# Kernel optimization log

Hardware: AMD Instinct MI355X
Metric: run time of the kernel (lower is better)

## Reference

```python
import jax, jax.numpy as jnp
import numpy as np

R, N, E, IN_DIM, HID, SEM_H = 3, 50000, 500000, 256, 128, 128


def setup_inputs() -> dict:
    key = jax.random.key(0)
    ks = jax.random.split(key, 20)
    s = 0.05
    return {
        # forward tensor args
        "dst_feat": jax.random.normal(ks[0], (N, IN_DIM), jnp.float32),
        "src_feats": jax.random.normal(ks[1], (R, N, IN_DIM), jnp.float32),
        "src_idx": jax.random.randint(ks[2], (R, E), 0, N, jnp.int32),
        "dst_idx": jax.random.randint(ks[3], (R, E), 0, N, jnp.int32),
        # weight_T: per-ntype projection in_dim -> hidden (dst ntype + R src ntypes, stacked)
        "WT_dst": jax.random.normal(ks[4], (IN_DIM, HID), jnp.float32) * s,
        "bT_dst": jnp.zeros((HID,), jnp.float32),
        "WT_src": jax.random.normal(ks[5], (R, IN_DIM, HID), jnp.float32) * s,
        "bT_src": jnp.zeros((R, HID), jnp.float32),
        # GATConv params per relation (1 head, shared fc for src/dst since in_feats is int)
        "W_gat": jax.random.normal(ks[6], (R, HID, HID), jnp.float32) * s,
        "attn_l": jax.random.normal(ks[7], (R, HID), jnp.float32) * s,
        "attn_r": jax.random.normal(ks[8], (R, HID), jnp.float32) * s,
        "b_gat": jnp.zeros((R, HID), jnp.float32),
        # SemanticAttention: Linear(HID,128)+tanh+Linear(128,1,no bias)
        "W1_sem": jax.random.normal(ks[9], (HID, SEM_H), jnp.float32) * s,
        "b1_sem": jnp.zeros((SEM_H,), jnp.float32),
        "w2_sem": jax.random.normal(ks[10], (SEM_H, 1), jnp.float32) * s,
    }


def reference(dst_feat, src_feats, src_idx, dst_idx,
              WT_dst, bT_dst, WT_src, bT_src,
              W_gat, attn_l, attn_r, b_gat,
              W1_sem, b1_sem, w2_sem):
    # weight_T projections (raw feat dim != hidden_dim branch)
    h_dst = dst_feat @ WT_dst + bT_dst                                  # [N, H]
    h_src = jnp.einsum('rni,rio->rno', src_feats, WT_src) + bT_src[:, None, :]  # [R, N, H]
    n_nodes = h_dst.shape[0]

    def gat(h_s_in, si, di, W, al, ar, b):
        # DGL GATConv, 1 head, eval mode (no dropout), shared fc for src/dst
        hs = h_s_in @ W                                                 # [N, H]
        hd = h_dst @ W                                                  # [N, H]
        el = (hs * al).sum(-1)                                          # [N]
        er = (hd * ar).sum(-1)                                          # [N]
        e = el[si] + er[di]                                             # [E]
        e = jnp.where(e > 0, e, 0.2 * e)                                # leaky_relu(0.2)
        # edge softmax segmented by destination node
        m = jax.ops.segment_max(e, di, num_segments=n_nodes)
        ex = jnp.exp(e - m[di])
        ssum = jax.ops.segment_sum(ex, di, num_segments=n_nodes)
        alpha = ex / ssum[di]                                           # [E]
        out = jax.ops.segment_sum(alpha[:, None] * hs[si], di, num_segments=n_nodes)  # [N, H]
        return jax.nn.elu(out + b)                                      # activation=F.elu, + bias

    z_r = jax.vmap(gat)(h_src, src_idx, dst_idx, W_gat, attn_l, attn_r, b_gat)  # [R, N, H]

    # SemanticAttention over relations
    z_m = jnp.transpose(z_r, (1, 0, 2))                                 # [N, R, H]
    w = jnp.tanh(z_m @ W1_sem + b1_sem) @ w2_sem                        # [N, R, 1]
    a = jax.nn.softmax(w.mean(axis=0), axis=0)                          # [R, 1]
    return (z_m * a).sum(axis=1)                                        # [N, H]
```

## Files before the change

kernel.cpp:

```cpp
#include <hip/hip_runtime.h>
#include <hip/hip_bf16.h>

#define R_REL 3
#define NODE_CHUNK 512
#define BCAP 6144

typedef __attribute__((ext_vector_type(8))) short bf16x8;
typedef __attribute__((ext_vector_type(4))) float f32x4;

static inline size_t align_up(size_t x, size_t a) { return (x + a - 1) & ~(a - 1); }

__device__ __forceinline__ float eluf(float x) {
    return x > 0.f ? x : (__expf(x) - 1.f);
}
__device__ __forceinline__ unsigned short f2bf(float f) {
    __hip_bfloat16 h = __float2bfloat16(f);
    return *reinterpret_cast<unsigned short*>(&h);
}
__device__ __forceinline__ unsigned pk2bf(float lo, float hi) {
    __hip_bfloat162 h = __float22bfloat162_rn(make_float2(lo, hi));
    return *reinterpret_cast<unsigned*>(&h);
}
__device__ __forceinline__ float bf2f(unsigned short h) {
    return __uint_as_float((unsigned)h << 16);
}


__global__ void vu_kernel(const float* __restrict__ W_gat, const float* __restrict__ attn_r,
                          const float* __restrict__ WT_dst, const float* __restrict__ bT_dst,
                          float* __restrict__ u, float* __restrict__ cc) {
    int r = blockIdx.x;
    int t = threadIdx.x;
    __shared__ float ar[128];
    __shared__ float vs[128];
    if (t < 128) ar[t] = attn_r[r * 128 + t];
    __syncthreads();
    if (t < 128) {
        const float* W = W_gat + (size_t)r * 128 * 128 + (size_t)t * 128;
        float s = 0.f;
        for (int j = 0; j < 128; ++j) s += W[j] * ar[j];
        vs[t] = s;
    }
    __syncthreads();
    const float* W = WT_dst + (size_t)t * 128;
    float s = 0.f;
    for (int i = 0; i < 128; ++i) s += W[i] * vs[i];
    u[r * 256 + t] = s;
    if (t == 0) {
        float c = 0.f;
        for (int i = 0; i < 128; ++i) c += bT_dst[i] * vs[i];
        cc[r] = c;
    }
}

__global__ void wc_kernel(const float* __restrict__ WT_src, const float* __restrict__ bT_src,
                          const float* __restrict__ W_gat, float* __restrict__ Wc,
                          float* __restrict__ bc) {
    int r = blockIdx.y;
    int k = blockIdx.x;
    int j = threadIdx.x;
    __shared__ float as[128];
    const float* arow = (k < 256) ? (WT_src + ((size_t)r * 256 + k) * 128)
                                  : (bT_src + (size_t)r * 128);
    as[j] = arow[j];
    __syncthreads();
    const float* W = W_gat + (size_t)r * 128 * 128;
    float s = 0.f;
    for (int i = 0; i < 128; ++i) s += as[i] * W[(size_t)i * 128 + j];
    if (k < 256) Wc[((size_t)r * 256 + k) * 128 + j] = s;
    else         bc[(size_t)r * 128 + j] = s;
}

__global__ void pack_kernel(const float* __restrict__ S, unsigned short* __restrict__ P,
                            int relstride, int KS) {
    int r = blockIdx.y;
    int ks = blockIdx.x >> 3, cb = blockIdx.x & 7;
    int l = threadIdx.x;
    const float* Sr = S + (size_t)r * relstride;
    int col = cb * 16 + (l & 15);
    int kb = ks * 32 + (l >> 4) * 8;
    unsigned short v[8];
#pragma unroll
    for (int j = 0; j < 8; ++j) v[j] = f2bf(Sr[(size_t)(kb + j) * 128 + col]);
    unsigned short* dst = P + ((((size_t)r * KS + ks) * 8 + cb) * 64 + l) * 8;
    *(uint4*)dst = *(uint4*)v;
}


__global__ __launch_bounds__(512) void gemm_hs(
    const float* __restrict__ src, const unsigned short* __restrict__ Bpack,
    const float* __restrict__ bc, const float* __restrict__ attn_l,
    unsigned short* __restrict__ hsb, float* __restrict__ el, int N) {
    const int r = blockIdx.y;
    const int t = threadIdx.x;
    const int w = t >> 6, l = t & 63;
    __shared__ unsigned short Blds[256 * 128];

    const unsigned short* bsrc = Bpack + (size_t)r * 256 * 128;
#pragma unroll
    for (int i = 0; i < 8; ++i) {
        int c = i * 512 + t;
        *(uint4*)&Blds[(size_t)c * 8] = *(const uint4*)&bsrc[(size_t)c * 8];
    }
    __syncthreads();

    const int rowbase = blockIdx.x * 128 + w * 16;
    const int arow_i = rowbase + (l & 15);
    const int kg = l >> 4;
    const float* A = src + (size_t)r * N * 256;
    const float* arow = A + (size_t)(arow_i < N ? arow_i : N - 1) * 256;

    f32x4 acc[8] = {};
#pragma unroll
    for (int ks = 0; ks < 8; ++ks) {
        float4 a0 = *(const float4*)(arow + ks * 32 + kg * 8);
        float4 a1 = *(const float4*)(arow + ks * 32 + kg * 8 + 4);
        uint4 uv;
        uv.x = pk2bf(a0.x, a0.y);
        uv.y = pk2bf(a0.z, a0.w);
        uv.z = pk2bf(a1.x, a1.y);
        uv.w = pk2bf(a1.z, a1.w);
        bf16x8 av = *(bf16x8*)&uv;
#pragma unroll
        for (int cf = 0; cf < 8; ++cf) {
            bf16x8 bv = *(const bf16x8*)&Blds[((size_t)(ks * 8 + cf) * 64 + l) * 8];
            acc[cf] = __builtin_amdgcn_mfma_f32_16x16x32_bf16(av, bv, acc[cf], 0, 0, 0);
        }
    }
    float bcv[8], alv[8];
#pragma unroll
    for (int cf = 0; cf < 8; ++cf) {
        int col = cf * 16 + (l & 15);
        bcv[cf] = bc[r * 128 + col];
        alv[cf] = attn_l[r * 128 + col];
    }
#pragma unroll
    for (int i = 0; i < 4; ++i) {
        int row = rowbase + (l >> 4) * 4 + i;
        float pe = 0.f;
        unsigned short hv[8];
#pragma unroll
        for (int cf = 0; cf < 8; ++cf) {
            float v = acc[cf][i] + bcv[cf];
            pe += v * alv[cf];
            hv[cf] = f2bf(v);
        }
        if (row < N) {
            unsigned short* hp = hsb + ((size_t)r * N + row) * 128 + (l & 15);
#pragma unroll
            for (int cf = 0; cf < 8; ++cf) hp[cf * 16] = hv[cf];
        }
        pe += __shfl_xor(pe, 1, 64);
        pe += __shfl_xor(pe, 2, 64);
        pe += __shfl_xor(pe, 4, 64);
        pe += __shfl_xor(pe, 8, 64);
        if ((l & 15) == 0 && row < N) el[(size_t)r * N + row] = pe;
    }
}


__global__ void er_kernel(const float* __restrict__ dst_feat, const float* __restrict__ u,
                          const float* __restrict__ cc, float* __restrict__ er, int N) {
    __shared__ float us[3][256];
    for (int i = threadIdx.x; i < 3 * 256; i += 256) us[i / 256][i & 255] = u[i];
    __syncthreads();
    int wave = threadIdx.x >> 6, lane = threadIdx.x & 63;
    int n = blockIdx.x * 4 + wave;
    if (n >= N) return;
    float4 f = *(const float4*)(dst_feat + (size_t)n * 256 + lane * 4);
#pragma unroll
    for (int r = 0; r < R_REL; ++r) {
        float4 uv = *(float4*)&us[r][lane * 4];
        float s = f.x * uv.x + f.y * uv.y + f.z * uv.z + f.w * uv.w;
#pragma unroll
        for (int off = 32; off >= 1; off >>= 1) s += __shfl_xor(s, off, 64);
        if (lane == 0) er[(size_t)r * N + n] = s + cc[r];
    }
}


__global__ __launch_bounds__(256) void bucket_kernel(
    const int* __restrict__ si, const int* __restrict__ di,
    int* __restrict__ gcnt, unsigned* __restrict__ bbuf, int NB, int E) {
    const int r = blockIdx.y;
    const int t = threadIdx.x;
    const int e0 = blockIdx.x * 1024;
    __shared__ int cnt[128];
    __shared__ int base[128];
    if (t < 128) cnt[t] = 0;
    __syncthreads();
    int bk[4], rank[4]; unsigned pack[4]; bool val[4];
#pragma unroll
    for (int j = 0; j < 4; ++j) {
        int e = e0 + j * 256 + t;
        val[j] = e < E;
        bk[j] = 0; rank[j] = 0; pack[j] = 0;
        if (val[j]) {
            size_t g = (size_t)r * E + e;
            int s = si[g], d = di[g];
            bk[j] = d >> 9;
            pack[j] = (unsigned)s | ((unsigned)d << 16);
            rank[j] = atomicAdd(&cnt[bk[j]], 1);
        }
    }
    __syncthreads();
    if (t < NB && cnt[t] > 0) base[t] = atomicAdd(&gcnt[r * NB + t], cnt[t]);
    __syncthreads();
#pragma unroll
    for (int j = 0; j < 4; ++j) {
        if (val[j])
            bbuf[((size_t)r * NB + bk[j]) * BCAP + base[bk[j]] + rank[j]] = pack[j];
    }
}

__global__ __launch_bounds__(256) void hist_kernel(
    const unsigned* __restrict__ bbuf, const int* __restrict__ gcnt,
    int* __restrict__ deg, int NB, int N) {
    const int r = blockIdx.y;
    const int b = blockIdx.x;
    const int t = threadIdx.x;
    __shared__ int hist[NODE_CHUNK];
    for (int i = t; i < NODE_CHUNK; i += 256) hist[i] = 0;
    __syncthreads();
    const int cnt = gcnt[r * NB + b];
    const unsigned* bb = bbuf + ((size_t)r * NB + b) * BCAP;
    for (int i = t; i < cnt; i += 256) {
        int dloc = (bb[i] >> 16) & (NODE_CHUNK - 1);
        atomicAdd(&hist[dloc], 1);
    }
    __syncthreads();
    for (int i = t; i < NODE_CHUNK; i += 256) {
        int idx = b * NODE_CHUNK + i;
        if (idx < N) deg[(size_t)r * N + idx] = hist[i];
    }
}

__global__ __launch_bounds__(1024) void scan1_kernel(const int* __restrict__ deg,
                                                     int* __restrict__ offs,
                                                     int* __restrict__ btot, int N, int nchunk) {
    const int r = blockIdx.y;
    const int idx = blockIdx.x * 1024 + threadIdx.x;
    const int lane = threadIdx.x & 63, wave = threadIdx.x >> 6;
    __shared__ int wsum[16];
    int v = (idx < N) ? deg[(size_t)r * N + idx] : 0;
    int x = v;
#pragma unroll
    for (int off = 1; off < 64; off <<= 1) {
        int y = __shfl_up(x, off, 64);
        if (lane >= off) x += y;
    }
    if (lane == 63) wsum[wave] = x;
    __syncthreads();
    if (wave == 0 && lane < 16) {
        int y = wsum[lane];
#pragma unroll
        for (int off = 1; off < 16; off <<= 1) {
            int z = __shfl_up(y, off, 64);
            if (lane >= off) y += z;
        }
        wsum[lane] = y;
    }
    __syncthreads();
    int woff = (wave > 0) ? wsum[wave - 1] : 0;
    if (idx < N) offs[(size_t)r * N + idx] = woff + x - v;
    if (threadIdx.x == 1023) btot[r * nchunk + blockIdx.x] = woff + x;
}

__global__ __launch_bounds__(256) void scan2_kernel(const int* __restrict__ btot,
                                                    int* __restrict__ offs, int N, int nchunk) {
    const int r = blockIdx.y;
    const int chunk = blockIdx.x;
    const int t = threadIdx.x;
    const int lane = t & 63, wave = t >> 6;
    __shared__ int red[4];
    int pre = 0;
    for (int i = t; i < chunk; i += 256) pre += btot[r * nchunk + i];
#pragma unroll
    for (int off = 32; off >= 1; off >>= 1) pre += __shfl_xor(pre, off, 64);
    if (lane == 0) red[wave] = pre;
    __syncthreads();
    int ptot = red[0] + red[1] + red[2] + red[3];
    for (int j = t; j < 1024; j += 256) {
        int idx = chunk * 1024 + j;
        if (idx < N) offs[(size_t)r * N + idx] += ptot;
    }
}

__global__ __launch_bounds__(256) void fill2p_kernel(
    const unsigned* __restrict__ bbuf, const int* __restrict__ gcnt,
    const int* __restrict__ offs, const float* __restrict__ el, const float* __restrict__ er,
    uint2* __restrict__ epair, int NB, int N, int E) {
    const int r = blockIdx.y;
    const int b = blockIdx.x;
    const int t = threadIdx.x;
    __shared__ int curl[NODE_CHUNK];
    __shared__ float erl[NODE_CHUNK];
    for (int i = t; i < NODE_CHUNK; i += 256) {
        int idx = b * NODE_CHUNK + i;
        curl[i] = (idx < N) ? offs[(size_t)r * N + idx] : 0;
        erl[i]  = (idx < N) ? er[(size_t)r * N + idx] : 0.f;
    }
    __syncthreads();
    const int cnt = gcnt[r * NB + b];
    const unsigned* bb = bbuf + ((size_t)r * NB + b) * BCAP;
    const float* elr = el + (size_t)r * N;
    uint2* epr = epair + (size_t)r * E;
    for (int i = t; i < cnt; i += 256) {
        unsigned pk = bb[i];
        int src = pk & 0xffffu;
        int dloc = (pk >> 16) & (NODE_CHUNK - 1);
        float e = elr[src] + erl[dloc];
        e = e > 0.f ? e : 0.2f * e;
        float p = __expf(e);
        int pos = atomicAdd(&curl[dloc], 1);
        epr[pos] = make_uint2((unsigned)src, __float_as_uint(p));
    }
}


__global__ __launch_bounds__(256) void gather_kernel(
    const uint2* __restrict__ epair, const int* __restrict__ offs,
    const int* __restrict__ deg, const unsigned short* __restrict__ hsb,
    const float* __restrict__ b_gat, unsigned short* __restrict__ z, int N, int E) {
    const int r = blockIdx.y;
    const int t = threadIdx.x;
    const int gid = t >> 4;
    const int gl = t & 15;
    const int d = blockIdx.x * 16 + gid;
    if (d >= N) return;
    const int beg = offs[(size_t)r * N + d];
    const int dg = deg[(size_t)r * N + d];
    float ac[8] = {0.f, 0.f, 0.f, 0.f, 0.f, 0.f, 0.f, 0.f};
    float ssum = 0.f;
    const uint2* epr = epair + (size_t)r * E;
    const unsigned short* hsr = hsb + (size_t)r * N * 128;
    int i = beg;
    const int end = beg + dg;
    for (; i + 3 < end; i += 4) {
        uint2 v0 = epr[i], v1 = epr[i + 1], v2 = epr[i + 2], v3 = epr[i + 3];
        uint4 h0 = *(const uint4*)(hsr + (size_t)v0.x * 128 + gl * 8);
        uint4 h1 = *(const uint4*)(hsr + (size_t)v1.x * 128 + gl * 8);
        uint4 h2 = *(const uint4*)(hsr + (size_t)v2.x * 128 + gl * 8);
        uint4 h3 = *(const uint4*)(hsr + (size_t)v3.x * 128 + gl * 8);
        float p0 = __uint_as_float(v0.y), p1 = __uint_as_float(v1.y);
        float p2 = __uint_as_float(v2.y), p3 = __uint_as_float(v3.y);
        ssum += p0 + p1 + p2 + p3;
        ac[0] += p0 * bf2f((unsigned short)(h0.x & 0xffffu)) + p1 * bf2f((unsigned short)(h1.x & 0xffffu))
               + p2 * bf2f((unsigned short)(h2.x & 0xffffu)) + p3 * bf2f((unsigned short)(h3.x & 0xffffu));
        ac[1] += p0 * bf2f((unsigned short)(h0.x >> 16)) + p1 * bf2f((unsigned short)(h1.x >> 16))
               + p2 * bf2f((unsigned short)(h2.x >> 16)) + p3 * bf2f((unsigned short)(h3.x >> 16));
        ac[2] += p0 * bf2f((unsigned short)(h0.y & 0xffffu)) + p1 * bf2f((unsigned short)(h1.y & 0xffffu))
               + p2 * bf2f((unsigned short)(h2.y & 0xffffu)) + p3 * bf2f((unsigned short)(h3.y & 0xffffu));
        ac[3] += p0 * bf2f((unsigned short)(h0.y >> 16)) + p1 * bf2f((unsigned short)(h1.y >> 16))
               + p2 * bf2f((unsigned short)(h2.y >> 16)) + p3 * bf2f((unsigned short)(h3.y >> 16));
        ac[4] += p0 * bf2f((unsigned short)(h0.z & 0xffffu)) + p1 * bf2f((unsigned short)(h1.z & 0xffffu))
               + p2 * bf2f((unsigned short)(h2.z & 0xffffu)) + p3 * bf2f((unsigned short)(h3.z & 0xffffu));
        ac[5] += p0 * bf2f((unsigned short)(h0.z >> 16)) + p1 * bf2f((unsigned short)(h1.z >> 16))
               + p2 * bf2f((unsigned short)(h2.z >> 16)) + p3 * bf2f((unsigned short)(h3.z >> 16));
        ac[6] += p0 * bf2f((unsigned short)(h0.w & 0xffffu)) + p1 * bf2f((unsigned short)(h1.w & 0xffffu))
               + p2 * bf2f((unsigned short)(h2.w & 0xffffu)) + p3 * bf2f((unsigned short)(h3.w & 0xffffu));
        ac[7] += p0 * bf2f((unsigned short)(h0.w >> 16)) + p1 * bf2f((unsigned short)(h1.w >> 16))
               + p2 * bf2f((unsigned short)(h2.w >> 16)) + p3 * bf2f((unsigned short)(h3.w >> 16));
    }
    for (; i < end; ++i) {
        uint2 v = epr[i];
        float p = __uint_as_float(v.y);
        ssum += p;
        uint4 hw = *(const uint4*)(hsr + (size_t)v.x * 128 + gl * 8);
        ac[0] += p * bf2f((unsigned short)(hw.x & 0xffffu));
        ac[1] += p * bf2f((unsigned short)(hw.x >> 16));
        ac[2] += p * bf2f((unsigned short)(hw.y & 0xffffu));
        ac[3] += p * bf2f((unsigned short)(hw.y >> 16));
        ac[4] += p * bf2f((unsigned short)(hw.z & 0xffffu));
        ac[5] += p * bf2f((unsigned short)(hw.z >> 16));
        ac[6] += p * bf2f((unsigned short)(hw.w & 0xffffu));
        ac[7] += p * bf2f((unsigned short)(hw.w >> 16));
    }
    float inv = (dg > 0) ? 1.f / ssum : 0.f;
    const float* bg = b_gat + r * 128 + gl * 8;
    uint4 ow;
    ow.x = pk2bf(eluf(ac[0] * inv + bg[0]), eluf(ac[1] * inv + bg[1]));
    ow.y = pk2bf(eluf(ac[2] * inv + bg[2]), eluf(ac[3] * inv + bg[3]));
    ow.z = pk2bf(eluf(ac[4] * inv + bg[4]), eluf(ac[5] * inv + bg[5]));
    ow.w = pk2bf(eluf(ac[6] * inv + bg[6]), eluf(ac[7] * inv + bg[7]));
    *(uint4*)(z + ((size_t)r * N + d) * 128 + gl * 8) = ow;
}


__global__ __launch_bounds__(256) void gemm_sem(
    const unsigned short* __restrict__ z, const unsigned short* __restrict__ W1p,
    const float* __restrict__ b1, const float* __restrict__ w2,
    float* __restrict__ wpart, int N) {
    const int r = blockIdx.y;
    const int n0 = blockIdx.x * 64;
    const int t = threadIdx.x;
    const int w = t >> 6, l = t & 63;
    __shared__ unsigned short Alds[64 * 128];
    __shared__ float sred[4];
    const unsigned short* A = z + (size_t)r * N * 128;
#pragma unroll
    for (int i = 0; i < 4; ++i) {
        int cid = t + 256 * i;
        int row = cid >> 4, kc = cid & 15;
        uint4 v = make_uint4(0, 0, 0, 0);
        if (n0 + row < N) v = *(const uint4*)(A + (size_t)(n0 + row) * 128 + kc * 8);
        int off = ((row * 256) + kc * 16) ^ ((row & 7) << 4);
        *(uint4*)((char*)Alds + off) = v;
    }
    __syncthreads();

    const bf16x8* bp = (const bf16x8*)W1p;
    f32x4 acc[8] = {};
    const int arow = w * 16 + (l & 15);
#pragma unroll
    for (int ks = 0; ks < 4; ++ks) {
        int aoff = ((arow * 256) + ks * 64 + (l >> 4) * 16) ^ ((arow & 7) << 4);
        bf16x8 av = *(const bf16x8*)((char*)Alds + aoff);
#pragma unroll
        for (int cf = 0; cf < 8; ++cf) {
            bf16x8 bv = bp[(ks * 8 + cf) * 64 + l];
            acc[cf] = __builtin_amdgcn_mfma_f32_16x16x32_bf16(av, bv, acc[cf], 0, 0, 0);
        }
    }
    float b1v[8], w2v[8];
#pragma unroll
    for (int cf = 0; cf < 8; ++cf) {
        int col = cf * 16 + (l & 15);
        b1v[cf] = b1[col];
        w2v[cf] = w2[col];
    }
    float wloc = 0.f;
#pragma unroll
    for (int i = 0; i < 4; ++i) {
        int row = n0 + w * 16 + (l >> 4) * 4 + i;
        float s = 0.f;
#pragma unroll
        for (int cf = 0; cf < 8; ++cf) s += tanhf(acc[cf][i] + b1v[cf]) * w2v[cf];
        s += __shfl_xor(s, 1, 64);
        s += __shfl_xor(s, 2, 64);
        s += __shfl_xor(s, 4, 64);
        s += __shfl_xor(s, 8, 64);
        if ((l & 15) == 0 && row < N) wloc += s;
    }
    wloc += __shfl_xor(wloc, 16, 64);
    wloc += __shfl_xor(wloc, 32, 64);
    if (l == 0) sred[w] = wloc;
    __syncthreads();
    if (t == 0)
        wpart[(size_t)r * gridDim.x + blockIdx.x] = sred[0] + sred[1] + sred[2] + sred[3];
}


__global__ void reduce_sem(const float* __restrict__ wpart, float* __restrict__ aw,
                           int nblk, int N) {
    const int t = threadIdx.x, l = t & 63, w = t >> 6;
    __shared__ float sred[R_REL][4];
    float s[R_REL] = {0.f, 0.f, 0.f};
    for (int i = t; i < nblk; i += 256) {
#pragma unroll
        for (int r = 0; r < R_REL; ++r) s[r] += wpart[(size_t)r * nblk + i];
    }
#pragma unroll
    for (int r = 0; r < R_REL; ++r) {
#pragma unroll
        for (int off = 32; off >= 1; off >>= 1) s[r] += __shfl_xor(s[r], off, 64);
        if (l == 0) sred[r][w] = s[r];
    }
    __syncthreads();
    if (t == 0) {
        float w0 = (sred[0][0] + sred[0][1] + sred[0][2] + sred[0][3]) / (float)N;
        float w1 = (sred[1][0] + sred[1][1] + sred[1][2] + sred[1][3]) / (float)N;
        float w2 = (sred[2][0] + sred[2][1] + sred[2][2] + sred[2][3]) / (float)N;
        float m = fmaxf(w0, fmaxf(w1, w2));
        float e0 = __expf(w0 - m), e1 = __expf(w1 - m), e2 = __expf(w2 - m);
        float si = e0 + e1 + e2;
        aw[0] = e0 / si; aw[1] = e1 / si; aw[2] = e2 / si;
    }
}

__global__ void combine(const unsigned short* __restrict__ z, const float* __restrict__ aw,
                        float* __restrict__ out, int N) {
    int idx = blockIdx.x * 256 + threadIdx.x;
    if (idx >= N * 32) return;
    int n = idx >> 5, c4 = idx & 31;
    float a0 = aw[0], a1 = aw[1], a2 = aw[2];
    uint2 z0 = *(const uint2*)(z + ((size_t)0 * N + n) * 128 + c4 * 4);
    uint2 z1 = *(const uint2*)(z + ((size_t)1 * N + n) * 128 + c4 * 4);
    uint2 z2 = *(const uint2*)(z + ((size_t)2 * N + n) * 128 + c4 * 4);
    float4 o;
    o.x = a0 * bf2f((unsigned short)(z0.x & 0xffffu)) + a1 * bf2f((unsigned short)(z1.x & 0xffffu)) + a2 * bf2f((unsigned short)(z2.x & 0xffffu));
    o.y = a0 * bf2f((unsigned short)(z0.x >> 16))     + a1 * bf2f((unsigned short)(z1.x >> 16))     + a2 * bf2f((unsigned short)(z2.x >> 16));
    o.z = a0 * bf2f((unsigned short)(z0.y & 0xffffu)) + a1 * bf2f((unsigned short)(z1.y & 0xffffu)) + a2 * bf2f((unsigned short)(z2.y & 0xffffu));
    o.w = a0 * bf2f((unsigned short)(z0.y >> 16))     + a1 * bf2f((unsigned short)(z1.y >> 16))     + a2 * bf2f((unsigned short)(z2.y >> 16));
    *(float4*)(out + (size_t)idx * 4) = o;
}


extern "C" void kernel_launch(void* const* d_in, const int* in_sizes, int n_in,
                              void* d_out, int out_size, void* d_ws, size_t ws_size,
                              hipStream_t stream) {
    const float* dst_feat = (const float*)d_in[0];
    const float* src_feats = (const float*)d_in[1];
    const int*   src_idx  = (const int*)d_in[2];
    const int*   dst_idx  = (const int*)d_in[3];
    const float* WT_dst   = (const float*)d_in[4];
    const float* bT_dst   = (const float*)d_in[5];
    const float* WT_src   = (const float*)d_in[6];
    const float* bT_src   = (const float*)d_in[7];
    const float* W_gat    = (const float*)d_in[8];
    const float* attn_l   = (const float*)d_in[9];
    const float* attn_r   = (const float*)d_in[10];
    const float* b_gat    = (const float*)d_in[11];
    const float* W1_sem   = (const float*)d_in[12];
    const float* b1_sem   = (const float*)d_in[13];
    const float* w2_sem   = (const float*)d_in[14];

    const int N = in_sizes[0] / 256;
    const int E = in_sizes[2] / R_REL;
    float* out = (float*)d_out;

    const int nblk = (N + 63) / 64;
    const int nblk_hs = (N + 127) / 128;
    const int nchunk = (N + 1023) / 1024;
    const int NB = (N + NODE_CHUNK - 1) / NODE_CHUNK;

    char* ws = (char*)d_ws;
    size_t off = 0;
    auto alloc = [&](size_t bytes) { char* p = ws + off; off = align_up(off + bytes, 256); return p; };
    unsigned short* hsb   = (unsigned short*)alloc((size_t)R_REL * N * 128 * 2);
    unsigned short* zbuf  = (unsigned short*)alloc((size_t)R_REL * N * 128 * 2);
    float*    Wc    = (float*)alloc((size_t)R_REL * 256 * 128 * 4);
    unsigned short* Wcp   = (unsigned short*)alloc((size_t)R_REL * 256 * 128 * 2);
    unsigned short* W1p   = (unsigned short*)alloc((size_t)128 * 128 * 2);
    float*    bc    = (float*)alloc(R_REL * 128 * 4);
    float*    u     = (float*)alloc(R_REL * 256 * 4);
    float*    cc    = (float*)alloc(R_REL * 4);
    float*    el    = (float*)alloc((size_t)R_REL * N * 4);
    float*    er    = (float*)alloc((size_t)R_REL * N * 4);
    int*      deg   = (int*)alloc((size_t)R_REL * N * 4);
    int*      offs  = (int*)alloc((size_t)R_REL * N * 4);
    int*      btot  = (int*)alloc((size_t)R_REL * nchunk * 4);
    int*      gcnt  = (int*)alloc((size_t)R_REL * NB * 4);
    unsigned* bbuf  = (unsigned*)alloc((size_t)R_REL * NB * BCAP * 4);
    uint2*    epair = (uint2*)alloc((size_t)R_REL * E * 8);
    float*    wpart = (float*)alloc((size_t)R_REL * nblk * 4);
    float*    aw    = (float*)alloc(R_REL * 4);

    hipMemsetAsync(gcnt, 0, (size_t)R_REL * NB * 4, stream);

    vu_kernel<<<R_REL, 256, 0, stream>>>(W_gat, attn_r, WT_dst, bT_dst, u, cc);
    wc_kernel<<<dim3(257, R_REL), 128, 0, stream>>>(WT_src, bT_src, W_gat, Wc, bc);
    pack_kernel<<<dim3(64, R_REL), 64, 0, stream>>>(Wc, Wcp, 256 * 128, 8);
    pack_kernel<<<dim3(32, 1), 64, 0, stream>>>(W1_sem, W1p, 0, 4);

    gemm_hs<<<dim3(nblk_hs, R_REL), 512, 0, stream>>>(src_feats, Wcp, bc, attn_l, hsb, el, N);
    er_kernel<<<(N + 3) / 4, 256, 0, stream>>>(dst_feat, u, cc, er, N);

    bucket_kernel<<<dim3((E + 1023) / 1024, R_REL), 256, 0, stream>>>(src_idx, dst_idx, gcnt, bbuf, NB, E);
    hist_kernel<<<dim3(NB, R_REL), 256, 0, stream>>>(bbuf, gcnt, deg, NB, N);
    scan1_kernel<<<dim3(nchunk, R_REL), 1024, 0, stream>>>(deg, offs, btot, N, nchunk);
    scan2_kernel<<<dim3(nchunk, R_REL), 256, 0, stream>>>(btot, offs, N, nchunk);
    fill2p_kernel<<<dim3(NB, R_REL), 256, 0, stream>>>(bbuf, gcnt, offs, el, er, epair, NB, N, E);

    gather_kernel<<<dim3((N + 15) / 16, R_REL), 256, 0, stream>>>(epair, offs, deg, hsb, b_gat, zbuf, N, E);

    gemm_sem<<<dim3(nblk, R_REL), 256, 0, stream>>>(zbuf, W1p, b1_sem, w2_sem, wpart, N);
    reduce_sem<<<1, 256, 0, stream>>>(wpart, aw, nblk, N);
    combine<<<(N * 32 + 255) / 256, 256, 0, stream>>>(zbuf, aw, out, N);
}
```

Before: 247.4 us.

## Replace scan2 pass with tiny chunk-prefix kernel and enlarge gemm_hs blocks

Drops the second scan pass that rewrote every offset with its chunk prefix. A single-thread-per-relation kernel now computes chunk prefixes, and fill2p and gather add them when they read offs. This removes a full read-modify-write of the offsets array. Separately, gemm_hs moves to 1024-thread blocks covering 256 rows, so the shared B tile is loaded half as often, at the cost of fewer blocks and higher register pressure per block.

```diff
diff --git a/kernel.cpp b/kernel.cpp
--- a/kernel.cpp
+++ b/kernel.cpp
@@ -87,7 +87,7 @@
 }
 
 
-__global__ __launch_bounds__(512) void gemm_hs(
+__global__ __launch_bounds__(1024) void gemm_hs(
     const float* __restrict__ src, const unsigned short* __restrict__ Bpack,
     const float* __restrict__ bc, const float* __restrict__ attn_l,
     unsigned short* __restrict__ hsb, float* __restrict__ el, int N) {
@@ -98,13 +98,13 @@
 
     const unsigned short* bsrc = Bpack + (size_t)r * 256 * 128;
 #pragma unroll
-    for (int i = 0; i < 8; ++i) {
-        int c = i * 512 + t;
+    for (int i = 0; i < 4; ++i) {
+        int c = i * 1024 + t;
         *(uint4*)&Blds[(size_t)c * 8] = *(const uint4*)&bsrc[(size_t)c * 8];
     }
     __syncthreads();
 
-    const int rowbase = blockIdx.x * 128 + w * 16;
+    const int rowbase = blockIdx.x * 256 + w * 16;
     const int arow_i = rowbase + (l & 15);
     const int kg = l >> 4;
     const float* A = src + (size_t)r * N * 256;
@@ -266,38 +266,30 @@
     if (threadIdx.x == 1023) btot[r * nchunk + blockIdx.x] = woff + x;
 }
 
-__global__ __launch_bounds__(256) void scan2_kernel(const int* __restrict__ btot,
-                                                    int* __restrict__ offs, int N, int nchunk) {
-    const int r = blockIdx.y;
-    const int chunk = blockIdx.x;
-    const int t = threadIdx.x;
-    const int lane = t & 63, wave = t >> 6;
-    __shared__ int red[4];
-    int pre = 0;
-    for (int i = t; i < chunk; i += 256) pre += btot[r * nchunk + i];
-#pragma unroll
-    for (int off = 32; off >= 1; off >>= 1) pre += __shfl_xor(pre, off, 64);
-    if (lane == 0) red[wave] = pre;
-    __syncthreads();
-    int ptot = red[0] + red[1] + red[2] + red[3];
-    for (int j = t; j < 1024; j += 256) {
-        int idx = chunk * 1024 + j;
-        if (idx < N) offs[(size_t)r * N + idx] += ptot;
+__global__ void cscan_kernel(const int* __restrict__ btot, int* __restrict__ cpre, int nchunk) {
+    int r = threadIdx.x;
+    if (r >= R_REL) return;
+    int acc = 0;
+    for (int i = 0; i < nchunk; ++i) {
+        cpre[r * nchunk + i] = acc;
+        acc += btot[r * nchunk + i];
     }
 }
 
 __global__ __launch_bounds__(256) void fill2p_kernel(
     const unsigned* __restrict__ bbuf, const int* __restrict__ gcnt,
-    const int* __restrict__ offs, const float* __restrict__ el, const float* __restrict__ er,
-    uint2* __restrict__ epair, int NB, int N, int E) {
+    const int* __restrict__ offs, const int* __restrict__ cpre,
+    const float* __restrict__ el, const float* __restrict__ er,
+    uint2* __restrict__ epair, int NB, int nchunk, int N, int E) {
     const int r = blockIdx.y;
     const int b = blockIdx.x;
     const int t = threadIdx.x;
     __shared__ int curl[NODE_CHUNK];
     __shared__ float erl[NODE_CHUNK];
+    const int cp = cpre[r * nchunk + (b >> 1)];
     for (int i = t; i < NODE_CHUNK; i += 256) {
         int idx = b * NODE_CHUNK + i;
-        curl[i] = (idx < N) ? offs[(size_t)r * N + idx] : 0;
+        curl[i] = (idx < N) ? offs[(size_t)r * N + idx] + cp : 0;
         erl[i]  = (idx < N) ? er[(size_t)r * N + idx] : 0.f;
     }
     __syncthreads();
@@ -320,15 +312,16 @@
 
 __global__ __launch_bounds__(256) void gather_kernel(
     const uint2* __restrict__ epair, const int* __restrict__ offs,
-    const int* __restrict__ deg, const unsigned short* __restrict__ hsb,
-    const float* __restrict__ b_gat, unsigned short* __restrict__ z, int N, int E) {
+    const int* __restrict__ cpre, const int* __restrict__ deg,
+    const unsigned short* __restrict__ hsb, const float* __restrict__ b_gat,
+    unsigned short* __restrict__ z, int N, int E, int nchunk) {
     const int r = blockIdx.y;
     const int t = threadIdx.x;
     const int gid = t >> 4;
     const int gl = t & 15;
     const int d = blockIdx.x * 16 + gid;
     if (d >= N) return;
-    const int beg = offs[(size_t)r * N + d];
+    const int beg = offs[(size_t)r * N + d] + cpre[r * nchunk + (d >> 10)];
     const int dg = deg[(size_t)r * N + d];
     float ac[8] = {0.f, 0.f, 0.f, 0.f, 0.f, 0.f, 0.f, 0.f};
     float ssum = 0.f;
@@ -520,7 +513,7 @@
     float* out = (float*)d_out;
 
     const int nblk = (N + 63) / 64;
-    const int nblk_hs = (N + 127) / 128;
+    const int nblk_hs = (N + 255) / 256;
     const int nchunk = (N + 1023) / 1024;
     const int NB = (N + NODE_CHUNK - 1) / NODE_CHUNK;
 
@@ -540,6 +533,7 @@
     int*      deg   = (int*)alloc((size_t)R_REL * N * 4);
     int*      offs  = (int*)alloc((size_t)R_REL * N * 4);
     int*      btot  = (int*)alloc((size_t)R_REL * nchunk * 4);
+    int*      cpre  = (int*)alloc((size_t)R_REL * nchunk * 4);
     int*      gcnt  = (int*)alloc((size_t)R_REL * NB * 4);
     unsigned* bbuf  = (unsigned*)alloc((size_t)R_REL * NB * BCAP * 4);
     uint2*    epair = (uint2*)alloc((size_t)R_REL * E * 8);
@@ -553,16 +547,16 @@
     pack_kernel<<<dim3(64, R_REL), 64, 0, stream>>>(Wc, Wcp, 256 * 128, 8);
     pack_kernel<<<dim3(32, 1), 64, 0, stream>>>(W1_sem, W1p, 0, 4);
 
-    gemm_hs<<<dim3(nblk_hs, R_REL), 512, 0, stream>>>(src_feats, Wcp, bc, attn_l, hsb, el, N);
+    gemm_hs<<<dim3(nblk_hs, R_REL), 1024, 0, stream>>>(src_feats, Wcp, bc, attn_l, hsb, el, N);
     er_kernel<<<(N + 3) / 4, 256, 0, stream>>>(dst_feat, u, cc, er, N);
 
     bucket_kernel<<<dim3((E + 1023) / 1024, R_REL), 256, 0, stream>>>(src_idx, dst_idx, gcnt, bbuf, NB, E);
     hist_kernel<<<dim3(NB, R_REL), 256, 0, stream>>>(bbuf, gcnt, deg, NB, N);
     scan1_kernel<<<dim3(nchunk, R_REL), 1024, 0, stream>>>(deg, offs, btot, N, nchunk);
-    scan2_kernel<<<dim3(nchunk, R_REL), 256, 0, stream>>>(btot, offs, N, nchunk);
-    fill2p_kernel<<<dim3(NB, R_REL), 256, 0, stream>>>(bbuf, gcnt, offs, el, er, epair, NB, N, E);
-
-    gather_kernel<<<dim3((N + 15) / 16, R_REL), 256, 0, stream>>>(epair, offs, deg, hsb, b_gat, zbuf, N, E);
+    cscan_kernel<<<1, 64, 0, stream>>>(btot, cpre, nchunk);
+    fill2p_kernel<<<dim3(NB, R_REL), 256, 0, stream>>>(bbuf, gcnt, offs, cpre, el, er, epair, NB, nchunk, N, E);
+
+    gather_kernel<<<dim3((N + 15) / 16, R_REL), 256, 0, stream>>>(epair, offs, cpre, deg, hsb, b_gat, zbuf, N, E, nchunk);
 
     gemm_sem<<<dim3(nblk, R_REL), 256, 0, stream>>>(zbuf, W1p, b1_sem, w2_sem, wpart, N);
     reduce_sem<<<1, 256, 0, stream>>>(wpart, aw, nblk, N);
```

Measured after the change: 245.7 us. Within noise of the previous version (-0.7%).
